# Performance work log

Hardware: AMD Instinct MI355X
Metric: run time of the kernel (lower is better)

The kernel has to match this reference:

```python
import jax, jax.numpy as jnp
import numpy as np

N, E, F_IN, H, L = 1536, 49152, 27, 64, 32


def _ln(x, g, b, eps=1e-5):
    m = x.mean(-1, keepdims=True)
    v = ((x - m) ** 2).mean(-1, keepdims=True)
    return (x - m) * jax.lax.rsqrt(v + eps) * g + b


def _gatv2(x, src, dst, Wl, bl, Wr, br, att, bias, n):
    # PyG GATv2Conv, heads=1: alpha_ij = softmax_j( att . leaky_relu(Wl x_j + Wr x_i) )
    xl = x @ Wl + bl  # source transform [n,H]
    xr = x @ Wr + br  # target transform [n,H]
    e = jax.nn.leaky_relu(xl[src] + xr[dst], 0.2)  # [E',H]
    s = e @ att  # [E'] attention logits
    m = jax.ops.segment_max(s, dst, num_segments=n)
    w = jnp.exp(s - m[dst])
    denom = jax.ops.segment_sum(w, dst, num_segments=n)
    alpha = w / denom[dst]
    return jax.ops.segment_sum(alpha[:, None] * xl[src], dst, num_segments=n) + bias


def _model(x, eps_nodes, eps_graph, edge_index,
           Wl1, bl1, Wr1, br1, att1, bias1,
           Wl2, bl2, Wr2, br2, att2, bias2,
           Wnm, bnm, Wnv, bnv, Wgm, bgm, Wgv, bgv,
           Wd1, bd1, ln1_g, ln1_b, Wd2, bd2, ln2_g, ln2_b, Wd3, bd3,
           We1, be1, lne_g, lne_b, We2, be2,
           Wf1, bf1, lnf_g, lnf_b, Wf2, bf2):
    n = x.shape[0]
    loop = jnp.arange(n)
    src = jnp.concatenate([edge_index[0], loop])  # add self loops (PyG default)
    dst = jnp.concatenate([edge_index[1], loop])
    h = jax.nn.relu(_gatv2(x, src, dst, Wl1, bl1, Wr1, br1, att1, bias1, n))
    h = jax.nn.relu(_gatv2(h, src, dst, Wl2, bl2, Wr2, br2, att2, bias2, n))
    node_mu = h @ Wnm + bnm
    node_logvar = h @ Wnv + bnv
    gh = h.mean(0)
    graph_mu = gh @ Wgm + bgm
    graph_logvar = gh @ Wgv + bgv
    z = node_mu + eps_nodes * jnp.exp(0.5 * node_logvar)  # node reparam (training)
    _zg = graph_mu + eps_graph * jnp.exp(0.5 * graph_logvar)  # z_graph: computed, unused downstream as in source
    # dec_node_features MLP
    nf = _ln(jax.nn.relu(z @ Wd1 + bd1), ln1_g, ln1_b)
    nf = _ln(jax.nn.relu(nf @ Wd2 + bd2), ln2_g, ln2_b)
    nf = nf @ Wd3 + bd3  # [n, F_IN]
    # feature_refinement (node_embeddings = h is passed in forward)
    nf = _ln(jax.nn.relu(jnp.concatenate([nf, h], -1) @ Wf1 + bf1), lnf_g, lnf_b)
    node_features = nf @ Wf2 + bf2
    # edge_pred over all i<j pairs, vectorized (replaces the O(N^2) python loop)
    iu, ju = jnp.triu_indices(n, k=1)
    ei = jnp.concatenate([z[iu], z[ju]], -1)  # [P, 2L]
    eh = _ln(jax.nn.relu(ei @ We1 + be1), lne_g, lne_b)
    edge_logits = (eh @ We2 + be2)[:, 0]  # [P]
    return node_features, edge_logits, node_mu, node_logvar, graph_mu, graph_logvar


def setup_inputs() -> dict:
    key = jax.random.key(0)
    ki = iter(jax.random.split(key, 40))
    def W(fi, fo):
        return jax.random.normal(next(ki), (fi, fo), jnp.float32) / np.sqrt(fi)
    z64 = jnp.zeros((H,), jnp.float32)
    o64 = jnp.ones((H,), jnp.float32)
    zL = jnp.zeros((L,), jnp.float32)
    zF = jnp.zeros((F_IN,), jnp.float32)
    inp = {}
    inp["x"] = jax.random.normal(next(ki), (N, F_IN), jnp.float32)
    inp["edge_index"] = jax.random.randint(next(ki), (2, E), 0, N)
    inp["eps_nodes"] = jax.random.normal(next(ki), (N, L), jnp.float32)
    inp["eps_graph"] = jax.random.normal(next(ki), (L,), jnp.float32)
    inp.update(Wl1=W(F_IN, H), bl1=z64, Wr1=W(F_IN, H), br1=z64,
               att1=jax.random.normal(next(ki), (H,), jnp.float32) / np.sqrt(H), bias1=z64,
               Wl2=W(H, H), bl2=z64, Wr2=W(H, H), br2=z64,
               att2=jax.random.normal(next(ki), (H,), jnp.float32) / np.sqrt(H), bias2=z64)
    inp.update(Wnm=W(H, L), bnm=zL, Wnv=W(H, L), bnv=zL,
               Wgm=W(H, L), bgm=zL, Wgv=W(H, L), bgv=zL)
    inp.update(Wd1=W(L, H), bd1=z64, ln1_g=o64, ln1_b=z64,
               Wd2=W(H, H), bd2=z64, ln2_g=o64, ln2_b=z64,
               Wd3=W(H, F_IN), bd3=zF)
    inp.update(We1=W(2 * L, H), be1=z64, lne_g=o64, lne_b=z64,
               We2=W(H, 1), be2=jnp.zeros((1,), jnp.float32))
    inp.update(Wf1=W(F_IN + H, H), bf1=z64, lnf_g=o64, lnf_b=z64,
               Wf2=W(H, F_IN), bf2=zF)
    return inp


def reference(x, edge_index, eps_nodes, eps_graph,
              Wl1, bl1, Wr1, br1, att1, bias1,
              Wl2, bl2, Wr2, br2, att2, bias2,
              Wnm, bnm, Wnv, bnv, Wgm, bgm, Wgv, bgv,
              Wd1, bd1, ln1_g, ln1_b, Wd2, bd2, ln2_g, ln2_b, Wd3, bd3,
              We1, be1, lne_g, lne_b, We2, be2,
              Wf1, bf1, lnf_g, lnf_b, Wf2, bf2):
    return _model(x, eps_nodes, eps_graph, edge_index,
                  Wl1, bl1, Wr1, br1, att1, bias1,
                  Wl2, bl2, Wr2, br2, att2, bias2,
                  Wnm, bnm, Wnv, bnv, Wgm, bgm, Wgv, bgv,
                  Wd1, bd1, ln1_g, ln1_b, Wd2, bd2, ln2_g, ln2_b, Wd3, bd3,
                  We1, be1, lne_g, lne_b, We2, be2,
                  Wf1, bf1, lnf_g, lnf_b, Wf2, bf2)
```

## Files before the change

### kernel.cpp

```cpp
#include <hip/hip_runtime.h>

#define NN 1536
#define NE 49152
#define FIN 27
#define HD 64
#define LDIM 32
#define PP 1178880
#define CAP 128
#define NTILE 1200

#define EL_OFF  (NN*FIN)
#define MU_OFF  (EL_OFF + PP)
#define LV_OFF  (MU_OFF + NN*LDIM)
#define GMU_OFF (LV_OFF + NN*LDIM)
#define GLV_OFF (GMU_OFF + LDIM)

__device__ __forceinline__ float wsum(float v) {
#pragma unroll
  for (int m = 1; m < 64; m <<= 1) v += __shfl_xor(v, m, 64);
  return v;
}
__device__ __forceinline__ void wsum2(float& a, float& b) {
#pragma unroll
  for (int m = 1; m < 64; m <<= 1) {
    a += __shfl_xor(a, m, 64);
    b += __shfl_xor(b, m, 64);
  }
}
__device__ __forceinline__ void wsum4(float& a, float& b, float& c, float& d) {
#pragma unroll
  for (int m = 1; m < 64; m <<= 1) {
    a += __shfl_xor(a, m, 64);
    b += __shfl_xor(b, m, 64);
    c += __shfl_xor(c, m, 64);
    d += __shfl_xor(d, m, 64);
  }
}
__device__ __forceinline__ float lnorm64(float x, float g, float b) {
  float s1 = x, s2 = x * x;
  wsum2(s1, s2);
  float mu = s1 * (1.0f / 64.0f);
  float var = fmaf(-mu, mu, s2 * (1.0f / 64.0f));
  return (x - mu) * rsqrtf(var + 1e-5f) * g + b;
}
__device__ __forceinline__ void cp4(float* dst, const float* __restrict__ src,
                                    int n4, int t) {
  const float4* s4 = (const float4*)src;
  float4* d4 = (float4*)dst;
  for (int e = t; e < n4; e += 256) d4[e] = s4[e];
}

__device__ __forceinline__ float gat_gather(const int* __restrict__ cnt,
                                            const int* __restrict__ slot,
                                            const float* __restrict__ xl,
                                            float xri, float ak, int i, int k) {
  int n = min(cnt[i], CAP);
  const int* srow = slot + i * CAP;
  float acc = 0.f, den = 0.f;
  for (int e0 = 0; e0 < n; e0 += 64) {
    int sidx = (e0 + k < n) ? srow[e0 + k] : 0;
    int nn = min(64, n - e0);
    int j = 0;
    for (; j + 3 < nn; j += 4) {
      int s0 = __shfl(sidx, j, 64),     s1 = __shfl(sidx, j + 1, 64);
      int s2 = __shfl(sidx, j + 2, 64), s3 = __shfl(sidx, j + 3, 64);
      float x0 = xl[s0 * HD + k], x1 = xl[s1 * HD + k];
      float x2 = xl[s2 * HD + k], x3 = xl[s3 * HD + k];
      float e0v = x0 + xri, e1v = x1 + xri, e2v = x2 + xri, e3v = x3 + xri;
      e0v = fmaxf(e0v, 0.2f * e0v);
      e1v = fmaxf(e1v, 0.2f * e1v);
      e2v = fmaxf(e2v, 0.2f * e2v);
      e3v = fmaxf(e3v, 0.2f * e3v);
      float p0 = e0v * ak, p1 = e1v * ak, p2 = e2v * ak, p3 = e3v * ak;
      wsum4(p0, p1, p2, p3);
      float w0 = expf(p0), w1 = expf(p1), w2 = expf(p2), w3 = expf(p3);
      acc = fmaf(w0, x0, acc); den += w0;
      acc = fmaf(w1, x1, acc); den += w1;
      acc = fmaf(w2, x2, acc); den += w2;
      acc = fmaf(w3, x3, acc); den += w3;
    }
    for (; j < nn; ++j) {
      int s0 = __shfl(sidx, j, 64);
      float x0 = xl[s0 * HD + k];
      float e0v = x0 + xri;
      e0v = fmaxf(e0v, 0.2f * e0v);
      float w0 = expf(wsum(e0v * ak));
      acc = fmaf(w0, x0, acc); den += w0;
    }
  }
  float xs = xl[i * HD + k];
  float es = xs + xri;
  es = fmaxf(es, 0.2f * es);
  float ws = expf(wsum(es * ak));
  acc = fmaf(ws, xs, acc); den += ws;
  return acc / den;
}

__global__ __launch_bounds__(256) void gvae_xform1(
    const float* __restrict__ in,
    const float* __restrict__ Wl, const float* __restrict__ bl,
    const float* __restrict__ Wr, const float* __restrict__ br,
    float* __restrict__ xl, float* __restrict__ xr,
    const int* __restrict__ ei, int* __restrict__ cnt, int* __restrict__ slot) {
  __shared__ __align__(16) float sWl[FIN * HD];
  __shared__ __align__(16) float sWr[FIN * HD];
  int t = threadIdx.x;
  int gid = blockIdx.x * 256 + t;
  if (gid < NE) {
    int d = ei[NE + gid];
    int c = atomicAdd(&cnt[d], 1);
    if (c < CAP) slot[d * CAP + c] = ei[gid];
  }
  cp4(sWl, Wl, FIN * 16, t);
  cp4(sWr, Wr, FIN * 16, t);
  int i = blockIdx.x * 4 + (t >> 6);
  int k = t & 63;
  float xv = (k < FIN) ? in[i * FIN + k] : 0.f;
  float l0 = bl[k], l1 = 0.f, r0 = br[k], r1 = 0.f;
  __syncthreads();
#pragma unroll
  for (int a = 0; a < FIN; a += 2) {
    float xa = __shfl(xv, a, 64);
    l0 = fmaf(xa, sWl[a * HD + k], l0);
    r0 = fmaf(xa, sWr[a * HD + k], r0);
    if (a + 1 < FIN) {
      float xb = __shfl(xv, a + 1, 64);
      l1 = fmaf(xb, sWl[(a + 1) * HD + k], l1);
      r1 = fmaf(xb, sWr[(a + 1) * HD + k], r1);
    }
  }
  xl[i * HD + k] = l0 + l1;
  xr[i * HD + k] = r0 + r1;
}

__global__ __launch_bounds__(256) void gvae_gatherx(
    const int* __restrict__ cnt, const int* __restrict__ slot,
    const float* __restrict__ xl, const float* __restrict__ xr,
    const float* __restrict__ att, const float* __restrict__ hbias,
    const float* __restrict__ Wl, const float* __restrict__ bl,
    const float* __restrict__ Wr, const float* __restrict__ br,
    float* __restrict__ xlo, float* __restrict__ xro) {
  int t = threadIdx.x;
  int i = blockIdx.x * 4 + (t >> 6);
  int k = t & 63;
  float xri = xr[i * HD + k];
  float ak = att[k];
  float hv = fmaxf(gat_gather(cnt, slot, xl, xri, ak, i, k) + hbias[k], 0.f);
  float l0 = bl[k], l1 = 0.f, r0 = br[k], r1 = 0.f;
#pragma unroll
  for (int a = 0; a < HD; a += 2) {
    float xa = __shfl(hv, a, 64);
    float xb = __shfl(hv, a + 1, 64);
    l0 = fmaf(xa, Wl[a * HD + k], l0);
    r0 = fmaf(xa, Wr[a * HD + k], r0);
    l1 = fmaf(xb, Wl[(a + 1) * HD + k], l1);
    r1 = fmaf(xb, Wr[(a + 1) * HD + k], r1);
  }
  xlo[i * HD + k] = l0 + l1;
  xro[i * HD + k] = r0 + r1;
}

__global__ __launch_bounds__(256, 4) void gvae_node(
    const int* __restrict__ cnt, const int* __restrict__ slot,
    const float* __restrict__ xl, const float* __restrict__ xr,
    const float* __restrict__ att, const float* __restrict__ bias2,
    const float* __restrict__ eps,
    const float* __restrict__ Wnm, const float* __restrict__ bnm,
    const float* __restrict__ Wnv, const float* __restrict__ bnv,
    const float* __restrict__ We1, const float* __restrict__ be1,
    float* __restrict__ uo, float* __restrict__ vo,
    float* __restrict__ h2o, float* __restrict__ zzo,
    float* __restrict__ gh, float* __restrict__ out) {
  __shared__ float ghred[256];
  int t = threadIdx.x;
  int i = blockIdx.x * 4 + (t >> 6);
  int k = t & 63;
  int kk = k & 31;

  float xri = xr[i * HD + k];
  float ak = att[k];
  float h2k = fmaxf(gat_gather(cnt, slot, xl, xri, ak, i, k) + bias2[k], 0.f);
  h2o[i * HD + k] = h2k;
  ghred[t] = h2k;
  __syncthreads();
  if (t < 64) {
    float s = (ghred[t] + ghred[t + 64]) + (ghred[t + 128] + ghred[t + 192]);
    atomicAdd(&gh[t], s * (1.0f / NN));
  }

  const float* W = (k < 32) ? Wnm : Wnv;
  float c0 = (k < 32) ? bnm[kk] : bnv[kk];
  float c1 = 0.f, c2 = 0.f, c3 = 0.f;
#pragma unroll
  for (int a = 0; a < HD; a += 4) {
    c0 = fmaf(__shfl(h2k, a, 64),     W[a * LDIM + kk],       c0);
    c1 = fmaf(__shfl(h2k, a + 1, 64), W[(a + 1) * LDIM + kk], c1);
    c2 = fmaf(__shfl(h2k, a + 2, 64), W[(a + 2) * LDIM + kk], c2);
    c3 = fmaf(__shfl(h2k, a + 3, 64), W[(a + 3) * LDIM + kk], c3);
  }
  float acc = (c0 + c1) + (c2 + c3);
  if (k < 32) out[MU_OFF + i * LDIM + kk] = acc;
  else        out[LV_OFF + i * LDIM + kk] = acc;

  float lv = __shfl(acc, k + 32, 64);
  float zk = acc + eps[i * LDIM + kk] * expf(0.5f * lv);
  if (k < 32) zzo[i * LDIM + kk] = zk;

  float u0 = be1[k], u1 = 0.f, v0 = 0.f, v1 = 0.f;
#pragma unroll
  for (int a = 0; a < LDIM; a += 2) {
    float za = __shfl(zk, a, 64);
    float zb = __shfl(zk, a + 1, 64);
    u0 = fmaf(za, We1[a * HD + k], u0);
    u1 = fmaf(zb, We1[(a + 1) * HD + k], u1);
    v0 = fmaf(za, We1[(a + LDIM) * HD + k], v0);
    v1 = fmaf(zb, We1[(a + 1 + LDIM) * HD + k], v1);
  }
  uo[i * HD + k] = u0 + u1;
  vo[i * HD + k] = v0 + v1;
}

__global__ __launch_bounds__(256) void gvae_edge(
    const float* __restrict__ u, const float* __restrict__ v,
    const float* __restrict__ lng, const float* __restrict__ lnb,
    const float* __restrict__ w2, const float* __restrict__ be2,
    const float* __restrict__ gh,
    const float* __restrict__ Wgm, const float* __restrict__ bgm,
    const float* __restrict__ Wgv, const float* __restrict__ bgv,
    const float* __restrict__ h2, const float* __restrict__ zz,
    const float* __restrict__ Wd1, const float* __restrict__ bd1,
    const float* __restrict__ g1, const float* __restrict__ b1,
    const float* __restrict__ Wd2, const float* __restrict__ bd2,
    const float* __restrict__ g2, const float* __restrict__ b2,
    const float* __restrict__ Wd3, const float* __restrict__ bd3,
    const float* __restrict__ Wf1, const float* __restrict__ bf1,
    const float* __restrict__ gf, const float* __restrict__ bfv,
    const float* __restrict__ Wf2, const float* __restrict__ bf2,
    float* __restrict__ out) {
  __shared__ float V[64 * 68];
  __shared__ float C[64];
  __shared__ float cc[2];
  int t = threadIdx.x;
  int b = blockIdx.x;
  int wv = t >> 6, lane = t & 63;

  if (b >= NTILE) {
    int i = (b - NTILE) * 4 + wv;
    int k = lane;
    int kc = (k < FIN) ? k : (FIN - 1);
    float h2k = h2[i * HD + k];
    float zk = zz[i * LDIM + (k & 31)];

    float c0 = bd1[k], c1 = 0.f, c2 = 0.f, c3 = 0.f;
#pragma unroll
    for (int a = 0; a < LDIM; a += 4) {
      c0 = fmaf(__shfl(zk, a, 64),     Wd1[a * HD + k],       c0);
      c1 = fmaf(__shfl(zk, a + 1, 64), Wd1[(a + 1) * HD + k], c1);
      c2 = fmaf(__shfl(zk, a + 2, 64), Wd1[(a + 2) * HD + k], c2);
      c3 = fmaf(__shfl(zk, a + 3, 64), Wd1[(a + 3) * HD + k], c3);
    }
    float nf1 = lnorm64(fmaxf((c0 + c1) + (c2 + c3), 0.f), g1[k], b1[k]);

    c0 = bd2[k]; c1 = 0.f; c2 = 0.f; c3 = 0.f;
#pragma unroll
    for (int a = 0; a < HD; a += 4) {
      c0 = fmaf(__shfl(nf1, a, 64),     Wd2[a * HD + k],       c0);
      c1 = fmaf(__shfl(nf1, a + 1, 64), Wd2[(a + 1) * HD + k], c1);
      c2 = fmaf(__shfl(nf1, a + 2, 64), Wd2[(a + 2) * HD + k], c2);
      c3 = fmaf(__shfl(nf1, a + 3, 64), Wd2[(a + 3) * HD + k], c3);
    }
    float nf2 = lnorm64(fmaxf((c0 + c1) + (c2 + c3), 0.f), g2[k], b2[k]);

    c0 = 0.f; c1 = 0.f; c2 = 0.f; c3 = 0.f;
#pragma unroll
    for (int a = 0; a < HD; a += 4) {
      c0 = fmaf(__shfl(nf2, a, 64),     Wd3[a * FIN + kc],       c0);
      c1 = fmaf(__shfl(nf2, a + 1, 64), Wd3[(a + 1) * FIN + kc], c1);
      c2 = fmaf(__shfl(nf2, a + 2, 64), Wd3[(a + 2) * FIN + kc], c2);
      c3 = fmaf(__shfl(nf2, a + 3, 64), Wd3[(a + 3) * FIN + kc], c3);
    }
    float nf3 = (k < FIN) ? ((c0 + c1) + (c2 + c3) + bd3[kc]) : 0.f;

    c0 = bf1[k]; c1 = 0.f; c2 = 0.f; c3 = 0.f;
#pragma unroll
    for (int j = 0; j < FIN; j++) {
      float nj = __shfl(nf3, j, 64);
      c0 = fmaf(nj, Wf1[j * HD + k], c0);
    }
#pragma unroll
    for (int a = 0; a < HD; a += 4) {
      c0 = fmaf(__shfl(h2k, a, 64),     Wf1[(FIN + a) * HD + k],     c0);
      c1 = fmaf(__shfl(h2k, a + 1, 64), Wf1[(FIN + a + 1) * HD + k], c1);
      c2 = fmaf(__shfl(h2k, a + 2, 64), Wf1[(FIN + a + 2) * HD + k], c2);
      c3 = fmaf(__shfl(h2k, a + 3, 64), Wf1[(FIN + a + 3) * HD + k], c3);
    }
    float rr = lnorm64(fmaxf((c0 + c1) + (c2 + c3), 0.f), gf[k], bfv[k]);

    c0 = 0.f; c1 = 0.f; c2 = 0.f; c3 = 0.f;
#pragma unroll
    for (int a = 0; a < HD; a += 4) {
      c0 = fmaf(__shfl(rr, a, 64),     Wf2[a * FIN + kc],       c0);
      c1 = fmaf(__shfl(rr, a + 1, 64), Wf2[(a + 1) * FIN + kc], c1);
      c2 = fmaf(__shfl(rr, a + 2, 64), Wf2[(a + 2) * FIN + kc], c2);
      c3 = fmaf(__shfl(rr, a + 3, 64), Wf2[(a + 3) * FIN + kc], c3);
    }
    if (k < FIN) out[i * FIN + k] = (c0 + c1) + (c2 + c3) + bf2[kc];
    return;
  }

  if (b == 0 && wv == 3) {
    int kk = lane & 31;
    float ghk = gh[lane];
    const float* W = (lane < 32) ? Wgm : Wgv;
    float c0 = (lane < 32) ? bgm[kk] : bgv[kk];
    float c1 = 0.f, c2 = 0.f, c3 = 0.f;
#pragma unroll
    for (int a = 0; a < HD; a += 4) {
      c0 = fmaf(__shfl(ghk, a, 64),     W[a * LDIM + kk],       c0);
      c1 = fmaf(__shfl(ghk, a + 1, 64), W[(a + 1) * LDIM + kk], c1);
      c2 = fmaf(__shfl(ghk, a + 2, 64), W[(a + 2) * LDIM + kk], c2);
      c3 = fmaf(__shfl(ghk, a + 3, 64), W[(a + 3) * LDIM + kk], c3);
    }
    float acc = (c0 + c1) + (c2 + c3);
    if (lane < 32) out[GMU_OFF + kk] = acc;
    else           out[GLV_OFF + kk] = acc;
  }

  int rem = b, cg = 0;
  while (rem >= 4 * (cg + 1)) { rem -= 4 * (cg + 1); cg++; }
  int rg = rem;

  float Ureg[4];
#pragma unroll
  for (int q = 0; q < 4; ++q)
    Ureg[q] = u[(rg * 16 + wv * 4 + q) * HD + lane];

  const float4* v4p = (const float4*)(v + cg * 64 * HD);
#pragma unroll
  for (int it = 0; it < 4; ++it) {
    int r = t + it * 256;
    int row = r >> 4, q = r & 15;
    float4 vv = v4p[r];
    *(float4*)&V[row * 68 + q * 4] = vv;
  }
  if (t < 64) {
    float ck = lng[t] * w2[t];
    C[t] = ck;
    float cb = lnb[t] * w2[t];
    float sC = wsum(ck);
    float sB = wsum(cb);
    if (t == 0) { cc[0] = sC; cc[1] = sB + be2[0]; }
  }
  __syncthreads();
  float C1 = cc[0], C0 = cc[1];

  float S1[4], S2[4], Sc[4];
#pragma unroll
  for (int q = 0; q < 4; q++) { S1[q] = 0.f; S2[q] = 0.f; Sc[q] = 0.f; }
  for (int k4 = 0; k4 < 16; k4++) {
    float4 v4 = *(const float4*)&V[lane * 68 + k4 * 4];
    float4 c4 = *(const float4*)&C[k4 * 4];
#pragma unroll
    for (int q = 0; q < 4; q++) {
      float u0 = __shfl(Ureg[q], k4 * 4, 64);
      float u1 = __shfl(Ureg[q], k4 * 4 + 1, 64);
      float u2 = __shfl(Ureg[q], k4 * 4 + 2, 64);
      float u3 = __shfl(Ureg[q], k4 * 4 + 3, 64);
      float t0 = fmaxf(u0 + v4.x, 0.f);
      float t1 = fmaxf(u1 + v4.y, 0.f);
      float t2 = fmaxf(u2 + v4.z, 0.f);
      float t3 = fmaxf(u3 + v4.w, 0.f);
      S1[q] += (t0 + t1) + (t2 + t3);
      S2[q] = fmaf(t0, t0, fmaf(t1, t1, fmaf(t2, t2, fmaf(t3, t3, S2[q]))));
      Sc[q] = fmaf(t0, c4.x, fmaf(t1, c4.y, fmaf(t2, c4.z, fmaf(t3, c4.w, Sc[q]))));
    }
  }
  int j = cg * 64 + lane;
  const float inv64 = 1.0f / 64.0f;
#pragma unroll
  for (int q = 0; q < 4; q++) {
    int i = rg * 16 + wv * 4 + q;
    if (j > i) {
      int pbase = i * (2 * NN - i - 1) / 2 - i - 1;
      float mu = S1[q] * inv64;
      float var = fmaf(-mu, mu, S2[q] * inv64);
      float logit = (Sc[q] - mu * C1) * rsqrtf(var + 1e-5f) + C0;
      out[EL_OFF + pbase + j] = logit;
    }
  }
}

extern "C" void kernel_launch(void* const* d_in, const int* in_sizes, int n_in,
                              void* d_out, int out_size, void* d_ws, size_t ws_size,
                              hipStream_t stream) {
  const float* x    = (const float*)d_in[0];
  const int*   ei   = (const int*)d_in[1];
  const float* eps  = (const float*)d_in[2];
  const float* Wl1  = (const float*)d_in[4];
  const float* bl1  = (const float*)d_in[5];
  const float* Wr1  = (const float*)d_in[6];
  const float* br1  = (const float*)d_in[7];
  const float* att1 = (const float*)d_in[8];
  const float* bias1= (const float*)d_in[9];
  const float* Wl2  = (const float*)d_in[10];
  const float* bl2  = (const float*)d_in[11];
  const float* Wr2  = (const float*)d_in[12];
  const float* br2  = (const float*)d_in[13];
  const float* att2 = (const float*)d_in[14];
  const float* bias2= (const float*)d_in[15];
  const float* Wnm  = (const float*)d_in[16];
  const float* bnm  = (const float*)d_in[17];
  const float* Wnv  = (const float*)d_in[18];
  const float* bnv  = (const float*)d_in[19];
  const float* Wgm  = (const float*)d_in[20];
  const float* bgm  = (const float*)d_in[21];
  const float* Wgv  = (const float*)d_in[22];
  const float* bgv  = (const float*)d_in[23];
  const float* Wd1  = (const float*)d_in[24];
  const float* bd1  = (const float*)d_in[25];
  const float* ln1g = (const float*)d_in[26];
  const float* ln1b = (const float*)d_in[27];
  const float* Wd2  = (const float*)d_in[28];
  const float* bd2  = (const float*)d_in[29];
  const float* ln2g = (const float*)d_in[30];
  const float* ln2b = (const float*)d_in[31];
  const float* Wd3  = (const float*)d_in[32];
  const float* bd3  = (const float*)d_in[33];
  const float* We1  = (const float*)d_in[34];
  const float* be1  = (const float*)d_in[35];
  const float* lneg = (const float*)d_in[36];
  const float* lneb = (const float*)d_in[37];
  const float* We2  = (const float*)d_in[38];
  const float* be2  = (const float*)d_in[39];
  const float* Wf1  = (const float*)d_in[40];
  const float* bf1  = (const float*)d_in[41];
  const float* lnfg = (const float*)d_in[42];
  const float* lnfb = (const float*)d_in[43];
  const float* Wf2  = (const float*)d_in[44];
  const float* bf2  = (const float*)d_in[45];
  float* out = (float*)d_out;

  float* fb  = (float*)d_ws;
  float* xl1 = fb;
  float* xr1 = xl1 + NN * HD;
  float* xl2 = xr1 + NN * HD;
  float* xr2 = xl2 + NN * HD;
  float* uu  = xr2 + NN * HD;
  float* vv  = uu  + NN * HD;
  float* h2  = vv  + NN * HD;
  float* zz  = h2  + NN * HD;
  float* gh  = zz  + NN * LDIM;
  int* cnt    = (int*)(gh + HD);
  int* slot   = cnt + NN;

  hipMemsetAsync(gh, 0, (HD + NN) * sizeof(float), stream);

  gvae_xform1<<<NN / 4, 256, 0, stream>>>(x, Wl1, bl1, Wr1, br1, xl1, xr1,
                                          ei, cnt, slot);
  gvae_gatherx<<<NN / 4, 256, 0, stream>>>(cnt, slot, xl1, xr1, att1, bias1,
                                           Wl2, bl2, Wr2, br2, xl2, xr2);
  gvae_node<<<NN / 4, 256, 0, stream>>>(cnt, slot, xl2, xr2, att2, bias2, eps,
      Wnm, bnm, Wnv, bnv, We1, be1,
      uu, vv, h2, zz, gh, out);
  gvae_edge<<<NTILE + NN / 4, 256, 0, stream>>>(uu, vv, lneg, lneb, We2, be2,
      gh, Wgm, bgm, Wgv, bgv,
      h2, zz,
      Wd1, bd1, ln1g, ln1b, Wd2, bd2, ln2g, ln2b, Wd3, bd3,
      Wf1, bf1, lnfg, lnfb, Wf2, bf2,
      out);
}
```

Measured before the change: 225.2 us.

## Split GAT neighbor gather across two wavefronts per node and shrink slot indices

```diff
diff --git a/kernel.cpp b/kernel.cpp
--- a/kernel.cpp
+++ b/kernel.cpp
@@ -50,18 +50,20 @@
   for (int e = t; e < n4; e += 256) d4[e] = s4[e];
 }
 
-__device__ __forceinline__ float gat_gather(const int* __restrict__ cnt,
-                                            const int* __restrict__ slot,
-                                            const float* __restrict__ xl,
-                                            float xri, float ak, int i, int k) {
+__device__ __forceinline__ void gat_gather_half(
+    const int* __restrict__ cnt, const unsigned short* __restrict__ slot,
+    const float* __restrict__ xl, float xri, float ak, int i, int k, int h,
+    float& accO, float& denO) {
   int n = min(cnt[i], CAP);
-  const int* srow = slot + i * CAP;
+  const unsigned short* srow = slot + i * CAP;
   float acc = 0.f, den = 0.f;
   for (int e0 = 0; e0 < n; e0 += 64) {
-    int sidx = (e0 + k < n) ? srow[e0 + k] : 0;
+    int sidx = (e0 + k < n) ? (int)srow[e0 + k] : 0;
     int nn = min(64, n - e0);
-    int j = 0;
-    for (; j + 3 < nn; j += 4) {
+    int jbeg = h * 32;
+    int jend = min(nn, jbeg + 32);
+    int j = jbeg;
+    for (; j + 3 < jend; j += 4) {
       int s0 = __shfl(sidx, j, 64),     s1 = __shfl(sidx, j + 1, 64);
       int s2 = __shfl(sidx, j + 2, 64), s3 = __shfl(sidx, j + 3, 64);
       float x0 = xl[s0 * HD + k], x1 = xl[s1 * HD + k];
@@ -79,7 +81,7 @@
       acc = fmaf(w2, x2, acc); den += w2;
       acc = fmaf(w3, x3, acc); den += w3;
     }
-    for (; j < nn; ++j) {
+    for (; j < jend; ++j) {
       int s0 = __shfl(sidx, j, 64);
       float x0 = xl[s0 * HD + k];
       float e0v = x0 + xri;
@@ -88,12 +90,14 @@
       acc = fmaf(w0, x0, acc); den += w0;
     }
   }
-  float xs = xl[i * HD + k];
-  float es = xs + xri;
-  es = fmaxf(es, 0.2f * es);
-  float ws = expf(wsum(es * ak));
-  acc = fmaf(ws, xs, acc); den += ws;
-  return acc / den;
+  if (h == 1) {
+    float xs = xl[i * HD + k];
+    float es = xs + xri;
+    es = fmaxf(es, 0.2f * es);
+    float ws = expf(wsum(es * ak));
+    acc = fmaf(ws, xs, acc); den += ws;
+  }
+  accO = acc; denO = den;
 }
 
 __global__ __launch_bounds__(256) void gvae_xform1(
@@ -101,7 +105,8 @@
     const float* __restrict__ Wl, const float* __restrict__ bl,
     const float* __restrict__ Wr, const float* __restrict__ br,
     float* __restrict__ xl, float* __restrict__ xr,
-    const int* __restrict__ ei, int* __restrict__ cnt, int* __restrict__ slot) {
+    const int* __restrict__ ei, int* __restrict__ cnt,
+    unsigned short* __restrict__ slot) {
   __shared__ __align__(16) float sWl[FIN * HD];
   __shared__ __align__(16) float sWr[FIN * HD];
   int t = threadIdx.x;
@@ -109,7 +114,7 @@
   if (gid < NE) {
     int d = ei[NE + gid];
     int c = atomicAdd(&cnt[d], 1);
-    if (c < CAP) slot[d * CAP + c] = ei[gid];
+    if (c < CAP) slot[d * CAP + c] = (unsigned short)ei[gid];
   }
   cp4(sWl, Wl, FIN * 16, t);
   cp4(sWr, Wr, FIN * 16, t);
@@ -133,35 +138,45 @@
   xr[i * HD + k] = r0 + r1;
 }
 
-__global__ __launch_bounds__(256) void gvae_gatherx(
-    const int* __restrict__ cnt, const int* __restrict__ slot,
+__global__ __launch_bounds__(512, 4) void gvae_gatherx(
+    const int* __restrict__ cnt, const unsigned short* __restrict__ slot,
     const float* __restrict__ xl, const float* __restrict__ xr,
     const float* __restrict__ att, const float* __restrict__ hbias,
     const float* __restrict__ Wl, const float* __restrict__ bl,
     const float* __restrict__ Wr, const float* __restrict__ br,
     float* __restrict__ xlo, float* __restrict__ xro) {
+  __shared__ float sA[4][2][64];
+  __shared__ float sD[4][2][64];
   int t = threadIdx.x;
-  int i = blockIdx.x * 4 + (t >> 6);
-  int k = t & 63;
+  int wv = t >> 6, k = t & 63;
+  int p = wv >> 1, h = wv & 1;
+  int i = blockIdx.x * 4 + p;
   float xri = xr[i * HD + k];
   float ak = att[k];
-  float hv = fmaxf(gat_gather(cnt, slot, xl, xri, ak, i, k) + hbias[k], 0.f);
-  float l0 = bl[k], l1 = 0.f, r0 = br[k], r1 = 0.f;
-#pragma unroll
-  for (int a = 0; a < HD; a += 2) {
-    float xa = __shfl(hv, a, 64);
-    float xb = __shfl(hv, a + 1, 64);
-    l0 = fmaf(xa, Wl[a * HD + k], l0);
-    r0 = fmaf(xa, Wr[a * HD + k], r0);
-    l1 = fmaf(xb, Wl[(a + 1) * HD + k], l1);
-    r1 = fmaf(xb, Wr[(a + 1) * HD + k], r1);
-  }
-  xlo[i * HD + k] = l0 + l1;
-  xro[i * HD + k] = r0 + r1;
-}
-
-__global__ __launch_bounds__(256, 4) void gvae_node(
-    const int* __restrict__ cnt, const int* __restrict__ slot,
+  float pa, pd;
+  gat_gather_half(cnt, slot, xl, xri, ak, i, k, h, pa, pd);
+  sA[p][h][k] = pa;
+  sD[p][h][k] = pd;
+  __syncthreads();
+  float hv = fmaxf((sA[p][0][k] + sA[p][1][k]) / (sD[p][0][k] + sD[p][1][k])
+                   + hbias[k], 0.f);
+  const float* W = h ? Wr : Wl;
+  float c0 = h ? br[k] : bl[k];
+  float c1 = 0.f, c2 = 0.f, c3 = 0.f;
+#pragma unroll
+  for (int a = 0; a < HD; a += 4) {
+    c0 = fmaf(__shfl(hv, a, 64),     W[a * HD + k],       c0);
+    c1 = fmaf(__shfl(hv, a + 1, 64), W[(a + 1) * HD + k], c1);
+    c2 = fmaf(__shfl(hv, a + 2, 64), W[(a + 2) * HD + k], c2);
+    c3 = fmaf(__shfl(hv, a + 3, 64), W[(a + 3) * HD + k], c3);
+  }
+  float r = (c0 + c1) + (c2 + c3);
+  if (h == 0) xlo[i * HD + k] = r;
+  else        xro[i * HD + k] = r;
+}
+
+__global__ __launch_bounds__(512, 4) void gvae_node(
+    const int* __restrict__ cnt, const unsigned short* __restrict__ slot,
     const float* __restrict__ xl, const float* __restrict__ xr,
     const float* __restrict__ att, const float* __restrict__ bias2,
     const float* __restrict__ eps,
@@ -171,53 +186,73 @@
     float* __restrict__ uo, float* __restrict__ vo,
     float* __restrict__ h2o, float* __restrict__ zzo,
     float* __restrict__ gh, float* __restrict__ out) {
+  __shared__ float sA[4][2][64];
+  __shared__ float sD[4][2][64];
+  __shared__ float sZ[4][32];
   __shared__ float ghred[256];
   int t = threadIdx.x;
-  int i = blockIdx.x * 4 + (t >> 6);
-  int k = t & 63;
+  int wv = t >> 6, k = t & 63;
+  int p = wv >> 1, h = wv & 1;
+  int i = blockIdx.x * 4 + p;
   int kk = k & 31;
 
   float xri = xr[i * HD + k];
   float ak = att[k];
-  float h2k = fmaxf(gat_gather(cnt, slot, xl, xri, ak, i, k) + bias2[k], 0.f);
-  h2o[i * HD + k] = h2k;
-  ghred[t] = h2k;
+  float pa, pd;
+  gat_gather_half(cnt, slot, xl, xri, ak, i, k, h, pa, pd);
+  sA[p][h][k] = pa;
+  sD[p][h][k] = pd;
+  __syncthreads();
+  float h2k = fmaxf((sA[p][0][k] + sA[p][1][k]) / (sD[p][0][k] + sD[p][1][k])
+                    + bias2[k], 0.f);
+  if (h == 0) {
+    h2o[i * HD + k] = h2k;
+    ghred[p * 64 + k] = h2k;
+  }
   __syncthreads();
   if (t < 64) {
     float s = (ghred[t] + ghred[t + 64]) + (ghred[t + 128] + ghred[t + 192]);
     atomicAdd(&gh[t], s * (1.0f / NN));
   }
 
-  const float* W = (k < 32) ? Wnm : Wnv;
-  float c0 = (k < 32) ? bnm[kk] : bnv[kk];
-  float c1 = 0.f, c2 = 0.f, c3 = 0.f;
-#pragma unroll
-  for (int a = 0; a < HD; a += 4) {
-    c0 = fmaf(__shfl(h2k, a, 64),     W[a * LDIM + kk],       c0);
-    c1 = fmaf(__shfl(h2k, a + 1, 64), W[(a + 1) * LDIM + kk], c1);
-    c2 = fmaf(__shfl(h2k, a + 2, 64), W[(a + 2) * LDIM + kk], c2);
-    c3 = fmaf(__shfl(h2k, a + 3, 64), W[(a + 3) * LDIM + kk], c3);
-  }
-  float acc = (c0 + c1) + (c2 + c3);
-  if (k < 32) out[MU_OFF + i * LDIM + kk] = acc;
-  else        out[LV_OFF + i * LDIM + kk] = acc;
-
-  float lv = __shfl(acc, k + 32, 64);
-  float zk = acc + eps[i * LDIM + kk] * expf(0.5f * lv);
-  if (k < 32) zzo[i * LDIM + kk] = zk;
-
-  float u0 = be1[k], u1 = 0.f, v0 = 0.f, v1 = 0.f;
-#pragma unroll
-  for (int a = 0; a < LDIM; a += 2) {
-    float za = __shfl(zk, a, 64);
-    float zb = __shfl(zk, a + 1, 64);
-    u0 = fmaf(za, We1[a * HD + k], u0);
-    u1 = fmaf(zb, We1[(a + 1) * HD + k], u1);
-    v0 = fmaf(za, We1[(a + LDIM) * HD + k], v0);
-    v1 = fmaf(zb, We1[(a + 1 + LDIM) * HD + k], v1);
-  }
-  uo[i * HD + k] = u0 + u1;
-  vo[i * HD + k] = v0 + v1;
+  if (h == 0) {
+    const float* W = (k < 32) ? Wnm : Wnv;
+    float c0 = (k < 32) ? bnm[kk] : bnv[kk];
+    float c1 = 0.f, c2 = 0.f, c3 = 0.f;
+#pragma unroll
+    for (int a = 0; a < HD; a += 4) {
+      c0 = fmaf(__shfl(h2k, a, 64),     W[a * LDIM + kk],       c0);
+      c1 = fmaf(__shfl(h2k, a + 1, 64), W[(a + 1) * LDIM + kk], c1);
+      c2 = fmaf(__shfl(h2k, a + 2, 64), W[(a + 2) * LDIM + kk], c2);
+      c3 = fmaf(__shfl(h2k, a + 3, 64), W[(a + 3) * LDIM + kk], c3);
+    }
+    float acc = (c0 + c1) + (c2 + c3);
+    if (k < 32) out[MU_OFF + i * LDIM + kk] = acc;
+    else        out[LV_OFF + i * LDIM + kk] = acc;
+
+    float lv = __shfl(acc, k + 32, 64);
+    float zk = acc + eps[i * LDIM + kk] * expf(0.5f * lv);
+    if (k < 32) {
+      zzo[i * LDIM + kk] = zk;
+      sZ[p][kk] = zk;
+    }
+  }
+  __syncthreads();
+  if (h == 1) {
+    float zk = sZ[p][kk];
+    float u0 = be1[k], u1 = 0.f, v0 = 0.f, v1 = 0.f;
+#pragma unroll
+    for (int a = 0; a < LDIM; a += 2) {
+      float za = __shfl(zk, a, 64);
+      float zb = __shfl(zk, a + 1, 64);
+      u0 = fmaf(za, We1[a * HD + k], u0);
+      u1 = fmaf(zb, We1[(a + 1) * HD + k], u1);
+      v0 = fmaf(za, We1[(a + LDIM) * HD + k], v0);
+      v1 = fmaf(zb, We1[(a + 1 + LDIM) * HD + k], v1);
+    }
+    uo[i * HD + k] = u0 + u1;
+    vo[i * HD + k] = v0 + v1;
+  }
 }
 
 __global__ __launch_bounds__(256) void gvae_edge(
@@ -451,15 +486,15 @@
   float* zz  = h2  + NN * HD;
   float* gh  = zz  + NN * LDIM;
   int* cnt    = (int*)(gh + HD);
-  int* slot   = cnt + NN;
+  unsigned short* slot = (unsigned short*)(cnt + NN);
 
   hipMemsetAsync(gh, 0, (HD + NN) * sizeof(float), stream);
 
   gvae_xform1<<<NN / 4, 256, 0, stream>>>(x, Wl1, bl1, Wr1, br1, xl1, xr1,
                                           ei, cnt, slot);
-  gvae_gatherx<<<NN / 4, 256, 0, stream>>>(cnt, slot, xl1, xr1, att1, bias1,
+  gvae_gatherx<<<NN / 4, 512, 0, stream>>>(cnt, slot, xl1, xr1, att1, bias1,
                                            Wl2, bl2, Wr2, br2, xl2, xr2);
-  gvae_node<<<NN / 4, 256, 0, stream>>>(cnt, slot, xl2, xr2, att2, bias2, eps,
+  gvae_node<<<NN / 4, 512, 0, stream>>>(cnt, slot, xl2, xr2, att2, bias2, eps,
       Wnm, bnm, Wnv, bnv, We1, be1,
       uu, vv, h2, zz, gh, out);
   gvae_edge<<<NTILE + NN / 4, 256, 0, stream>>>(uu, vv, lneg, lneb, We2, be2,
```

Result: faster. 219.7 us (-2.4%).
